# Kernel tuning notes

Measured on AMD Instinct MI355X. Metric: run time of the kernel, lower is better.

## Reference

```python
import jax, jax.numpy as jnp
import numpy as np

S = 1024; VOCAB = 100000; EMB = 300
POS_SZ = 64; CHAR_E = 50; CHAR_ENC = 128; WLEN = 16
NCHARS = 100; NPOSTAG = 50; NPOSITIONS = 1024
D = EMB + 3 * POS_SZ + CHAR_ENC  # word_rep_size = 620
BIH = 128   # per-direction LSTM hidden (bilstm_hidden_size // 2)
TLH = 256; LCC = 128; GCC = 256
NET = 8; NTAGS = 16; NREL = 16
TOKF = 2 * BIH + LCC + TLH       # 640
SENTF = 2 * TOKF + GCC           # 1536

def _p(k, shape):
    return 0.02 * jax.random.normal(k, shape, dtype=jnp.float32)

def setup_inputs():
    key = jax.random.key(0)
    ks = jax.random.split(key, 30)
    return {
        'word_inputs': jax.random.randint(ks[0], (1, S), 0, VOCAB),
        'char_inputs': jax.random.randint(ks[1], (1, S, WLEN), 0, NCHARS),
        'postag_inputs': jax.random.randint(ks[2], (1, S), 0, NPOSTAG),
        'dependency_inputs': jax.random.randint(ks[3], (1, S), 0, 64),
        'position_inputs': jax.random.randint(ks[4], (1, S), 0, NPOSITIONS),
        'topo_order': jnp.arange(S),  # children-before-parents order
        'parent': jnp.concatenate([jnp.arange(1, S), jnp.array([S])]),  # chain dep tree; root -> dummy slot S
        'pointed_token_idx': 5,
        'word_table': _p(ks[5], (VOCAB, EMB)),
        'char_table': _p(ks[6], (NCHARS, CHAR_E)),
        'char_conv_w': _p(ks[7], (CHAR_ENC, CHAR_E, 3)),
        'char_conv_b': jnp.zeros((CHAR_ENC,), jnp.float32),
        'postag_table': _p(ks[8], (NPOSTAG, POS_SZ)),
        'position_table': _p(ks[9], (NPOSITIONS, POS_SZ)),
        'lstm_f_Wx': _p(ks[10], (D, 4 * BIH)),
        'lstm_f_Wh': _p(ks[11], (BIH, 4 * BIH)),
        'lstm_f_b': jnp.zeros((4 * BIH,), jnp.float32),
        'lstm_b_Wx': _p(ks[12], (D, 4 * BIH)),
        'lstm_b_Wh': _p(ks[13], (BIH, 4 * BIH)),
        'lstm_b_b': jnp.zeros((4 * BIH,), jnp.float32),
        'word_cnn_w': _p(ks[14], (LCC, D, 3)),
        'word_cnn_b': jnp.zeros((LCC,), jnp.float32),
        'tl_Wiou': _p(ks[15], (D, 3 * TLH)),
        'tl_Uiou': _p(ks[16], (TLH, 3 * TLH)),
        'tl_biou': jnp.zeros((3 * TLH,), jnp.float32),
        'tl_Wf': _p(ks[17], (D, TLH)),
        'tl_Uf': _p(ks[18], (TLH, TLH)),
        'tl_bf': jnp.zeros((TLH,), jnp.float32),
        'sent_cnn_w': _p(ks[19], (GCC, D, 3)),
        'sent_cnn_b': jnp.zeros((GCC,), jnp.float32),
        'et_w': _p(ks[20], (GCC + TOKF, NET)),
        'et_b': jnp.zeros((NET,), jnp.float32),
        'crf_w': _p(ks[21], (SENTF, NTAGS)),
        'crf_b': jnp.zeros((NTAGS,), jnp.float32),
        'crf_trans': _p(ks[22], (NTAGS, NTAGS)),
        'rel_w': _p(ks[23], (SENTF, NREL)),
        'rel_b': jnp.zeros((NREL,), jnp.float32),
    }

def _conv1d(x, w, b):
    # x: [N, Cin, W], w: [Cout, Cin, K], padding=1 (matches nn.Conv1d(..., padding=1))
    y = jax.lax.conv_general_dilated(x, w, (1,), [(1, 1)], dimension_numbers=('NCW', 'OIW', 'NCW'))
    return y + b[None, :, None]

def _lstm(xs, Wx, Wh, b):
    H = Wh.shape[0]
    def step(carry, x):
        h, c = carry
        g = x @ Wx + h @ Wh + b
        i, f, gg, o = jnp.split(g, 4, axis=-1)
        c = jax.nn.sigmoid(f) * c + jax.nn.sigmoid(i) * jnp.tanh(gg)
        h = jax.nn.sigmoid(o) * jnp.tanh(c)
        return (h, c), h
    init = (jnp.zeros((H,), xs.dtype), jnp.zeros((H,), xs.dtype))
    _, hs = jax.lax.scan(step, init, xs)
    return hs

def _tree_lstm(x, order, parent, Wiou, Uiou, biou, Wf, Uf, bf):
    # ChildSum TreeLSTM over the whole dependency tree in topological order.
    # Equivalent to the source's per-token subtree recursion: each node's h
    # only depends on its subtree.
    Sn, H = x.shape[0], Uf.shape[0]
    xiou = x @ Wiou + biou                 # [S, 3H]
    xf = jnp.concatenate([x @ Wf + bf, jnp.zeros((1, H), x.dtype)], axis=0)  # dummy row for root's parent
    def step(carry, j):
        h, hsum, fcsum = carry
        iou = xiou[j] + hsum[j] @ Uiou
        i, o, u = jnp.split(iou, 3)
        cj = jax.nn.sigmoid(i) * jnp.tanh(u) + fcsum[j]
        hj = jax.nn.sigmoid(o) * jnp.tanh(cj)
        p = parent[j]
        f = jax.nn.sigmoid(xf[p] + hj @ Uf)  # per-child forget gate
        return (h.at[j].set(hj), hsum.at[p].add(hj), fcsum.at[p].add(f * cj)), None
    h0 = jnp.zeros((Sn, H), x.dtype)
    acc0 = jnp.zeros((Sn + 1, H), x.dtype)
    (h, _, _), _ = jax.lax.scan(step, (h0, acc0, acc0), order)
    return h

def _viterbi(emissions, trans):
    # emissions: [S, T]; trans[i, j] = score(i -> j)
    def step(score, e):
        s = score[:, None] + trans
        return jnp.max(s, axis=0) + e, jnp.argmax(s, axis=0)
    final, ptrs = jax.lax.scan(step, emissions[0], emissions[1:])
    last = jnp.argmax(final)
    def bt(tag, p):
        prev = p[tag]
        return prev, prev
    _, prevs = jax.lax.scan(bt, last, ptrs, reverse=True)
    return jnp.concatenate([prevs, last[None]])

def reference(word_inputs, char_inputs, postag_inputs, dependency_inputs, position_inputs, topo_order, parent, pointed_token_idx, word_table, char_table, char_conv_w, char_conv_b, postag_table, position_table, lstm_f_Wx, lstm_f_Wh, lstm_f_b, lstm_b_Wx, lstm_b_Wh, lstm_b_b, word_cnn_w, word_cnn_b, tl_Wiou, tl_Uiou, tl_biou, tl_Wf, tl_Uf, tl_bf, sent_cnn_w, sent_cnn_b, et_w, et_b, crf_w, crf_b, crf_trans, rel_w, rel_b):
    we = word_table[word_inputs]                                   # [1,S,EMB]
    cx = jnp.transpose(char_table[char_inputs[0]], (0, 2, 1))      # [S,CHAR_E,WLEN]
    ce = jnp.max(jax.nn.relu(_conv1d(cx, char_conv_w, char_conv_b)), axis=-1)[None]  # CharCNN -> [1,S,CHAR_ENC]
    pe = postag_table[postag_inputs]
    poe = position_table[position_inputs]
    de = position_table[dependency_inputs]                         # faithful to source bug: uses position table
    inputs = jnp.concatenate([we, ce, pe, poe, de], axis=-1)       # [1,S,D]
    x = inputs[0]
    hf = _lstm(x, lstm_f_Wx, lstm_f_Wh, lstm_f_b)
    hb = _lstm(x[::-1], lstm_b_Wx, lstm_b_Wh, lstm_b_b)[::-1]
    bilstm = jnp.concatenate([hf, hb], axis=-1)[None]              # [1,S,2*BIH]
    xc = jnp.transpose(inputs, (0, 2, 1))                          # [1,D,S]
    local_cnn = jnp.transpose(_conv1d(xc, word_cnn_w, word_cnn_b), (0, 2, 1))
    tree_h = _tree_lstm(x, topo_order, parent, tl_Wiou, tl_Uiou, tl_biou, tl_Wf, tl_Uf, tl_bf)[None]
    global_cnn = jnp.transpose(jnp.max(_conv1d(xc, sent_cnn_w, sent_cnn_b), axis=-1, keepdims=True), (0, 2, 1))  # [1,1,GCC]
    tokens_info = jnp.concatenate([bilstm, local_cnn, tree_h], axis=-1)  # [1,S,TOKF]
    ptr = tokens_info[:, pointed_token_idx, :]                     # [1,TOKF]
    ptr_info = jnp.broadcast_to(ptr[:, None, :], (1, S, TOKF))
    glob_info = jnp.broadcast_to(global_cnn, (1, S, GCC))
    sentence_encoding = jnp.concatenate([tokens_info, ptr_info, glob_info], axis=-1)  # dropout = identity (eval)
    one_vec = jnp.concatenate([global_cnn[:, 0, :], ptr], axis=-1)
    entitytype = jax.nn.softmax(one_vec @ et_w + et_b, axis=-1)
    entities = _viterbi(sentence_encoding[0] @ crf_w + crf_b, crf_trans)
    relations = jax.nn.sigmoid(sentence_encoding @ rel_w + rel_b)
    return sentence_encoding, entitytype, entities, relations
```

## Files before the change

kernel.cpp:

```cpp
#include <hip/hip_runtime.h>
#include <math.h>

#define SEQ   1024
#define DX    620
#define BIH   128
#define TLH   256
#define NTAGS 16

#define O_X      0
#define O_XGF    634880
#define O_XGB    (O_XGF + 524288)
#define O_XIOU   (O_XGB + 524288)
#define O_XF     (O_XIOU + 786432)
#define O_LCNN   (O_XF + 262400)
#define O_SCNN   (O_LCNN + 131072)
#define O_PART   (O_SCNN + 262144)
#define O_GCNN   (O_PART + 4096)
#define O_HF     (O_GCNN + 256)
#define O_HB     (O_HF + 131072)
#define O_TREEH  (O_HB + 131072)
#define O_IOUA   (O_TREEH + 262144)
#define O_FCSUM  (O_IOUA + 787200)
#define O_EMIS   (O_FCSUM + 262400)
#define O_CNT    (O_EMIS + 16384)

#define C_XGF  0
#define C_XGB  16
#define C_XIOU 32
#define C_XF   48
#define C_X    64
#define C_SCNN 80

#define SENT 0xFFFFFFFFu

__device__ __forceinline__ float sig_f(float x){ return 1.0f/(1.0f + __expf(-x)); }
__device__ __forceinline__ float tanh_f(float x){
  float ax = fabsf(x);
  float e  = __expf(-2.0f*ax);
  float t  = (1.0f - e)/(1.0f + e);
  return x < 0.0f ? -t : t;
}
__device__ __forceinline__ int physslot(int s){ return s ^ ((s>>3)&7); }

__device__ __forceinline__ void wait_cnt(int* cnt, int idx, int target){
  while (__hip_atomic_load(&cnt[idx], __ATOMIC_ACQUIRE, __HIP_MEMORY_SCOPE_AGENT) < target)
    __builtin_amdgcn_s_sleep(8);
}

__device__ __forceinline__ void gemm_tile(
    const float* __restrict__ x, const float* __restrict__ Bm,
    const float* __restrict__ bias, float* __restrict__ C,
    int N, int K, int amode, int bx, int by, int tid,
    float (*As)[64], float (*Bs)[64], int agentc)
{
  int bn = bx*64, bm = by*64;
  int lane = tid & 63, kg = tid >> 6;
  int tx = tid & 15, ty = tid >> 4;
  float acc[4][4] = {{0.f}};
  for (int k0 = 0; k0 < K; k0 += 20){
    #pragma unroll
    for (int kk=0; kk<5; kk++){
      int k = kg*5 + kk;
      float av;
      if (amode == 0){
        av = x[(size_t)(bm+lane)*DX + k0 + k];
      } else {
        int kc = k0 + k;
        int d  = kc/3;
        int sh = kc - d*3 - 1;
        int row = bm + lane + sh;
        av = (row >= 0 && row < SEQ) ? x[(size_t)row*DX + d] : 0.0f;
      }
      As[k][lane] = av;
      Bs[k][lane] = (amode==0) ? Bm[(size_t)(k0+k)*N + bn + lane]
                               : Bm[(size_t)(bn+lane)*K + k0 + k];
    }
    __syncthreads();
    #pragma unroll
    for (int k=0;k<20;k++){
      float4 a = *(const float4*)&As[k][ty<<2];
      float4 b = *(const float4*)&Bs[k][tx<<2];
      acc[0][0]+=a.x*b.x; acc[0][1]+=a.x*b.y; acc[0][2]+=a.x*b.z; acc[0][3]+=a.x*b.w;
      acc[1][0]+=a.y*b.x; acc[1][1]+=a.y*b.y; acc[1][2]+=a.y*b.z; acc[1][3]+=a.y*b.w;
      acc[2][0]+=a.z*b.x; acc[2][1]+=a.z*b.y; acc[2][2]+=a.z*b.z; acc[2][3]+=a.z*b.w;
      acc[3][0]+=a.w*b.x; acc[3][1]+=a.w*b.y; acc[3][2]+=a.w*b.z; acc[3][3]+=a.w*b.w;
    }
    __syncthreads();
  }
  float4 bb;
  bb.x = bias[bn+(tx<<2)+0]; bb.y = bias[bn+(tx<<2)+1];
  bb.z = bias[bn+(tx<<2)+2]; bb.w = bias[bn+(tx<<2)+3];
  #pragma unroll
  for (int i=0;i<4;i++){
    int row = bm + (ty<<2) + i;
    float v0 = acc[i][0]+bb.x, v1 = acc[i][1]+bb.y, v2 = acc[i][2]+bb.z, v3 = acc[i][3]+bb.w;
    if (agentc){
      float* p = &C[(size_t)row*N + bn + (tx<<2)];
      __hip_atomic_store(p+0, v0, __ATOMIC_RELAXED, __HIP_MEMORY_SCOPE_AGENT);
      __hip_atomic_store(p+1, v1, __ATOMIC_RELAXED, __HIP_MEMORY_SCOPE_AGENT);
      __hip_atomic_store(p+2, v2, __ATOMIC_RELAXED, __HIP_MEMORY_SCOPE_AGENT);
      __hip_atomic_store(p+3, v3, __ATOMIC_RELAXED, __HIP_MEMORY_SCOPE_AGENT);
    } else {
      float4 o; o.x=v0; o.y=v1; o.z=v2; o.w=v3;
      *(float4*)&C[(size_t)row*N + bn + (tx<<2)] = o;
    }
  }
}

struct RGemm {
  const float* B[4];
  const float* bias[4];
  float*       C[4];
  int          N[4];
};

__global__ __launch_bounds__(256, 1) void k_recur(
    const int* __restrict__ wi, const int* __restrict__ ci,
    const int* __restrict__ postag_in, const int* __restrict__ dep_in, const int* __restrict__ pos_in,
    const float* __restrict__ word_table, const float* __restrict__ char_table,
    const float* __restrict__ ccw, const float* __restrict__ ccb,
    const float* __restrict__ postag_tab, const float* __restrict__ pos_tab,
    const float* __restrict__ xg_f, const float* __restrict__ xg_b,
    const float* __restrict__ Wh_f, const float* __restrict__ Wh_b,
    const float* __restrict__ xiou, const float* __restrict__ xf,
    const float* __restrict__ Uiou, const float* __restrict__ Uf,
    const int* __restrict__ order, const int* __restrict__ parent,
    float* __restrict__ hf, float* __restrict__ hb,
    float* tree_h, float* iou_acc, float* fcsum,
    float* __restrict__ x, RGemm rg_args,
    const float* __restrict__ wcnn_w, const float* __restrict__ wcnn_b,
    const float* __restrict__ scnn_w, const float* __restrict__ scnn_b,
    float* __restrict__ lcnn, float* __restrict__ scnn, float* __restrict__ gcnn,
    int* cnt)
{
  int bid = blockIdx.x;
  int tid = threadIdx.x;

  if (bid >= 775){
    __shared__ __align__(16) float As[20][64];
    __shared__ __align__(16) float Bs[20][64];
    int j = bid - 775;
    for (int s=0;s<3;s++){
      int tn = j*3 + s;
      int by = (tn < 32) ? (tn>>1) : ((tn-32)>>2);
      if (tid == 0){
        int glo = by > 0 ? by-1 : 0, ghi = by < 15 ? by+1 : 15;
        for (int g = glo; g <= ghi; g++) wait_cnt(cnt, C_X + g, 32);
      }
      __syncthreads();
      if (tn < 32){
        gemm_tile(x, wcnn_w, wcnn_b, lcnn, 128, 1860, 1, tn&1, by, tid, As, Bs, 0);
      } else {
        int t2 = tn - 32;
        gemm_tile(x, scnn_w, scnn_b, scnn, 256, 1860, 1, t2&3, by, tid, As, Bs, 0);
        __syncthreads();
        if (tid == 0)
          __hip_atomic_fetch_add(&cnt[C_SCNN], 1, __ATOMIC_RELEASE, __HIP_MEMORY_SCOPE_AGENT);
      }
      __syncthreads();
    }
    return;
  }

  if (bid >= 519){
    __shared__ __align__(16) float As[20][64];
    __shared__ __align__(16) float Bs[20][64];
    int j = bid - 519;
    for (int s=0;s<2;s++){
      int T = j*2 + s;
      int k = T>>5, r = T&31;
      int z, by, bn;
      if (r < 8)       { z=0; by=k;    bn=r;    }
      else if (r < 16) { z=1; by=15-k; bn=r-8;  }
      else if (r < 28) { z=2; by=k;    bn=r-16; }
      else             { z=3; by=k;    bn=r-28; }
      if (tid == 0) wait_cnt(cnt, C_X + by, 32);
      __syncthreads();
      gemm_tile(x, rg_args.B[z], rg_args.bias[z], rg_args.C[z], rg_args.N[z],
                620, 0, bn, by, tid, As, Bs, 1);
      __syncthreads();
      if (tid == 0)
        __hip_atomic_fetch_add(&cnt[z*16 + by], 1, __ATOMIC_RELEASE, __HIP_MEMORY_SCOPE_AGENT);
      __syncthreads();
    }
    return;
  }

  if (bid >= 7){
    int j   = bid - 7;
    int tok = j*2 + (tid >> 7);
    int lt  = tid & 127;
    __shared__ __align__(16) float ce2[2][50][16];
    float (*ce)[16] = ce2[tid >> 7];
    for (int idx = lt; idx < 800; idx += 128){
      int e = idx >> 4, t = idx & 15;
      ce[e][t] = char_table[ci[tok*16 + t]*50 + e];
    }
    __syncthreads();
    float* xr = x + (size_t)tok*DX;
    const float* wrow = word_table + (size_t)wi[tok]*300;
    for (int d = lt; d < 300; d += 128) xr[d] = wrow[d];
    {
      int oc = lt;
      const float* wp = ccw + oc*150;
      float acc[16];
      float b = ccb[oc];
      #pragma unroll
      for (int t=0;t<16;t++) acc[t] = b;
      for (int ic=0; ic<50; ic++){
        float w0 = wp[ic*3+0], w1 = wp[ic*3+1], w2 = wp[ic*3+2];
        float cv[16];
        float4 c0 = *(const float4*)&ce[ic][0];
        float4 c1 = *(const float4*)&ce[ic][4];
        float4 c2 = *(const float4*)&ce[ic][8];
        float4 c3 = *(const float4*)&ce[ic][12];
        cv[0]=c0.x;cv[1]=c0.y;cv[2]=c0.z;cv[3]=c0.w;
        cv[4]=c1.x;cv[5]=c1.y;cv[6]=c1.z;cv[7]=c1.w;
        cv[8]=c2.x;cv[9]=c2.y;cv[10]=c2.z;cv[11]=c2.w;
        cv[12]=c3.x;cv[13]=c3.y;cv[14]=c3.z;cv[15]=c3.w;
        #pragma unroll
        for (int t=0;t<16;t++){
          float a = cv[t]*w1;
          if (t > 0)  a += cv[t-1]*w0;
          if (t < 15) a += cv[t+1]*w2;
          acc[t] += a;
        }
      }
      float m = acc[0];
      #pragma unroll
      for (int t=1;t<16;t++) m = fmaxf(m, acc[t]);
      xr[300 + oc] = fmaxf(m, 0.0f);
    }
    if (lt < 64){
      int d = lt;
      xr[428 + d] = postag_tab[postag_in[tok]*64 + d];
      xr[492 + d] = pos_tab[pos_in[tok]*64 + d];
      xr[556 + d] = pos_tab[dep_in[tok]*64 + d];
    }
    __syncthreads();
    if (tid == 0)
      __hip_atomic_fetch_add(&cnt[C_X + ((j*2) >> 6)], 1, __ATOMIC_RELEASE, __HIP_MEMORY_SCOPE_AGENT);
    return;
  }

  if (bid == 6){
    if (tid == 0) wait_cnt(cnt, C_SCNN, 64);
    __syncthreads();
    int c = tid;
    float m = -3.0e38f;
    #pragma unroll 8
    for (int s = 0; s < SEQ; s++) m = fmaxf(m, scnn[(size_t)s*256 + c]);
    gcnn[c] = m;
    return;
  }

  if (bid >= 4){
    const float* xg  = (bid == 4) ? xg_f : xg_b;
    const float* Wh  = (bid == 4) ? Wh_f : Wh_b;
    float* hout      = (bid == 4) ? hf : hb;
    int zc = (bid == 4) ? 0 : 1;
    int cg = tid >> 1, rg = tid & 1;
    float4 w[4][16];
    #pragma unroll
    for (int cc=0;cc<4;cc++){
      int col = cg*4 + cc;
      #pragma unroll
      for (int r4=0;r4<16;r4++){
        int row = rg*64 + r4*4;
        w[cc][r4].x = Wh[(size_t)(row+0)*512 + col];
        w[cc][r4].y = Wh[(size_t)(row+1)*512 + col];
        w[cc][r4].z = Wh[(size_t)(row+2)*512 + col];
        w[cc][r4].w = Wh[(size_t)(row+3)*512 + col];
      }
    }
    #pragma unroll
    for (int cc=0;cc<4;cc++)
      #pragma unroll
      for (int r4=0;r4<16;r4++)
        asm volatile("" : "+v"(w[cc][r4].x), "+v"(w[cc][r4].y), "+v"(w[cc][r4].z), "+v"(w[cc][r4].w));

    __shared__ __align__(16) float lhl[BIH];
    __shared__ float lcst[BIH];
    __shared__ float gl[512];
    if (tid < BIH){ lhl[tid] = 0.f; lcst[tid] = 0.f; }
    __syncthreads();
    const float4* lhl4 = (const float4*)lhl;

    int Wm = (bid == 4) ? -1 : 16;
    {
      int n0 = (bid == 4) ? 0 : (SEQ-1);
      int g0 = n0 >> 6;
      if (tid == 0){
        if (bid == 4){ for (int g = 0; g <= g0; g++) wait_cnt(cnt, zc*16+g, 8); }
        else         { for (int g = 15; g >= g0; g--) wait_cnt(cnt, zc*16+g, 8); }
      }
      __syncthreads();
      Wm = g0;
    }
    float4 nxg4 = make_float4(0.f,0.f,0.f,0.f);
    if (rg == 0){
      int n0 = (bid == 4) ? 0 : (SEQ-1);
      nxg4 = *(const float4*)&xg[(size_t)n0*512 + cg*4];
    }
    for (int st=0; st<SEQ; st++){
      int n = (bid == 4) ? st : (SEQ-1-st);
      float4 xg4 = nxg4;
      if (st+1 < SEQ){
        int n1 = (bid == 4) ? (st+1) : (SEQ-2-st);
        int g1 = n1 >> 6;
        if (g1 != Wm){
          if (tid == 0) wait_cnt(cnt, zc*16+g1, 8);
          __syncthreads();
          Wm = g1;
        }
        if (rg == 0) nxg4 = *(const float4*)&xg[(size_t)n1*512 + cg*4];
      }
      float acc[4] = {0.f,0.f,0.f,0.f};
      #pragma unroll
      for (int r4=0;r4<16;r4++){
        float4 h4 = lhl4[rg*16 + r4];
        #pragma unroll
        for (int cc=0;cc<4;cc++)
          acc[cc] += h4.x*w[cc][r4].x + h4.y*w[cc][r4].y + h4.z*w[cc][r4].z + h4.w*w[cc][r4].w;
      }
      #pragma unroll
      for (int cc=0;cc<4;cc++) acc[cc] += __shfl_xor(acc[cc], 1);
      if (rg == 0){
        float4 o = make_float4(acc[0]+xg4.x, acc[1]+xg4.y, acc[2]+xg4.z, acc[3]+xg4.w);
        *(float4*)&gl[cg*4] = o;
      }
      __syncthreads();
      if (tid < BIH){
        float gi = gl[tid], gf = gl[BIH+tid], gg = gl[2*BIH+tid], go = gl[3*BIH+tid];
        float c = sig_f(gf)*lcst[tid] + sig_f(gi)*tanh_f(gg);
        float h = sig_f(go)*tanh_f(c);
        lcst[tid] = c;
        lhl[tid] = h;
        hout[(size_t)n*BIH + tid] = h;
      }
      __syncthreads();
    }
    return;
  }

  int blk = bid;
  int cg = tid >> 3, rg = tid & 7;
  int ulo = blk*64;
  float4 w[8][8];
  #pragma unroll
  for (int cc=0;cc<8;cc++){
    int c = cg*8 + cc;
    const float* Wsrc; size_t stride; int gcol;
    if (c < 192){ Wsrc = Uiou; stride = 768; gcol = (c>>6)*TLH + ulo + (c&63); }
    else        { Wsrc = Uf;   stride = 256; gcol = ulo + (c-192); }
    #pragma unroll
    for (int r4=0;r4<8;r4++){
      int row = rg*32 + r4*4;
      w[cc][r4].x = Wsrc[(size_t)(row+0)*stride + gcol];
      w[cc][r4].y = Wsrc[(size_t)(row+1)*stride + gcol];
      w[cc][r4].z = Wsrc[(size_t)(row+2)*stride + gcol];
      w[cc][r4].w = Wsrc[(size_t)(row+3)*stride + gcol];
    }
  }
  #pragma unroll
  for (int cc=0;cc<8;cc++)
    #pragma unroll
    for (int r4=0;r4<8;r4++)
      asm volatile("" : "+v"(w[cc][r4].x), "+v"(w[cc][r4].y), "+v"(w[cc][r4].z), "+v"(w[cc][r4].w));

  __shared__ __align__(16) float hl[TLH];
  __shared__ float colsum[TLH];
  __shared__ float cprev[64];
  __shared__ int ord_l[SEQ];
  __shared__ int par_l[SEQ];
  for (int i=tid; i<SEQ; i+=256){ ord_l[i] = order[i]; par_l[i] = parent[i]; }
  __syncthreads();
  const float4* hl4 = (const float4*)hl;

  int Wm = -1;
  float nxi=0.f, nxo=0.f, nxu=0.f, nxf=0.f;
  {
    int n0 = ord_l[0];
    int need = n0 >> 6;
    if (tid == 0){
      for (int g = 0; g <= need; g++){
        wait_cnt(cnt, C_XIOU + g, 12);
        wait_cnt(cnt, C_XF + g, 4);
      }
    }
    __syncthreads();
    Wm = need;
    if (tid < 64){
      int uu = ulo + tid;
      nxi = xiou[(size_t)n0*768 + uu];
      nxo = xiou[(size_t)n0*768 + 256 + uu];
      nxu = xiou[(size_t)n0*768 + 512 + uu];
    }
  }

  for (int t=0; t<SEQ; t++){
    int n  = ord_l[t];
    int m  = (t > 0) ? ord_l[t-1] : 0;
    int pp = (t > 0) ? par_l[m] : -1;
    bool ppeq = (pp == n);

    int need = -1;
    if (t+1 < SEQ){
      int n1 = ord_l[t+1];
      int pr = par_l[n];
      need = n1 >> 6;
      if (pr < SEQ && (pr>>6) > need) need = pr>>6;
      if (need > Wm){
        if (tid == 0){
          for (int g = Wm+1; g <= need; g++){
            wait_cnt(cnt, C_XIOU + g, 12);
            wait_cnt(cnt, C_XF + g, 4);
          }
        }
        __syncthreads();
        Wm = need;
      }
    }

    float xi=nxi, xo=nxo, xu=nxu, xfv=nxf;
    float ac_i=0.f, ac_o=0.f, ac_u=0.f, fcn=0.f;
    float po_i=0.f, po_o=0.f, po_u=0.f, po_f=0.f;
    if (tid < 64){
      int uu = ulo + tid;
      if (t+1 < SEQ){
        int n1 = ord_l[t+1];
        int pr = par_l[n];
        nxi = xiou[(size_t)n1*768 + uu];
        nxo = xiou[(size_t)n1*768 + 256 + uu];
        nxu = xiou[(size_t)n1*768 + 512 + uu];
        nxf = xf[(size_t)pr*256 + uu];
      }
      ac_i = iou_acc[(size_t)n*768 + uu];
      ac_o = iou_acc[(size_t)n*768 + 256 + uu];
      ac_u = iou_acc[(size_t)n*768 + 512 + uu];
      fcn  = fcsum[(size_t)n*256 + uu];
      if (t > 0 && !ppeq){
        po_i = iou_acc[(size_t)pp*768 + uu];
        po_o = iou_acc[(size_t)pp*768 + 256 + uu];
        po_u = iou_acc[(size_t)pp*768 + 512 + uu];
        po_f = fcsum[(size_t)pp*256 + uu];
      }
    }

    if (t > 0){
      float acc[8] = {0.f,0.f,0.f,0.f,0.f,0.f,0.f,0.f};
      int base = rg << 3;
      #pragma unroll
      for (int r4=0;r4<8;r4++){
        float4 h4 = hl4[base + (r4 ^ rg)];
        #pragma unroll
        for (int cc=0;cc<8;cc++)
          acc[cc] += h4.x*w[cc][r4].x + h4.y*w[cc][r4].y + h4.z*w[cc][r4].z + h4.w*w[cc][r4].w;
      }
      #pragma unroll
      for (int cc=0;cc<8;cc++){
        acc[cc] += __shfl_xor(acc[cc], 1);
        acc[cc] += __shfl_xor(acc[cc], 2);
        acc[cc] += __shfl_xor(acc[cc], 4);
      }
      if (rg == 0){
        *(float4*)&colsum[cg*8]     = make_float4(acc[0], acc[1], acc[2], acc[3]);
        *(float4*)&colsum[cg*8 + 4] = make_float4(acc[4], acc[5], acc[6], acc[7]);
      }
    }
    __syncthreads();

    if (tid < 64){
      int uu = ulo + tid;
      float ai = ac_i, ao = ac_o, au = ac_u, fcs = fcn;
      if (t > 0){
        float vi = colsum[tid], vo = colsum[64+tid], vuu = colsum[128+tid], vf = colsum[192+tid];
        float fg  = sig_f(xfv + vf);
        float fcc = fg * cprev[tid];
        if (ppeq){
          ai += vi; ao += vo; au += vuu; fcs += fcc;
        } else {
          iou_acc[(size_t)pp*768 + uu]       = po_i + vi;
          iou_acc[(size_t)pp*768 + 256 + uu] = po_o + vo;
          iou_acc[(size_t)pp*768 + 512 + uu] = po_u + vuu;
          fcsum[(size_t)pp*256 + uu]         = po_f + fcc;
        }
      }
      float cc = sig_f(xi + ai)*tanh_f(xu + au) + fcs;
      float hh = sig_f(xo + ao)*tanh_f(cc);
      cprev[tid] = cc;
      int s = uu >> 2;
      hl[physslot(s)*4 + (uu & 3)] = hh;
      __hip_atomic_store(&tree_h[(size_t)n*TLH + uu], hh, __ATOMIC_RELAXED, __HIP_MEMORY_SCOPE_AGENT);
    } else if (tid >= 64 && tid < 256){
      int p  = tid - 64;
      int fi = (p < ulo) ? p : p + 64;
      const unsigned* tp = (const unsigned*)(tree_h + (size_t)n*TLH + fi);
      unsigned v = __hip_atomic_load(tp, __ATOMIC_RELAXED, __HIP_MEMORY_SCOPE_AGENT);
      while (v == SENT){
        __builtin_amdgcn_s_sleep(1);
        v = __hip_atomic_load(tp, __ATOMIC_RELAXED, __HIP_MEMORY_SCOPE_AGENT);
      }
      hl[physslot(fi>>2)*4 + (fi&3)] = __uint_as_float(v);
    }
    __syncthreads();
  }
}

__global__ __launch_bounds__(256) void k_assemble(
    const float* __restrict__ hf, const float* __restrict__ hb,
    const float* __restrict__ lcnn, const float* __restrict__ tree_h,
    const float* __restrict__ gcnn,
    const float* __restrict__ crf_w, const float* __restrict__ crf_b,
    const float* __restrict__ rel_w, const float* __restrict__ rel_b,
    const float* __restrict__ et_w, const float* __restrict__ et_b,
    const int* __restrict__ ptk,
    float* __restrict__ se_out, float* __restrict__ emis, float* __restrict__ rel_out,
    float* __restrict__ out_et)
{
  int tid = threadIdx.x;
  int p = ptk[0];
  if (blockIdx.x == SEQ){
    __shared__ float ov[896];
    __shared__ float lg[8];
    for (int d = tid; d < 896; d += 256){
      float v;
      if      (d < 256) v = gcnn[d];
      else if (d < 384) v = hf[(size_t)p*128 + d-256];
      else if (d < 512) v = hb[(size_t)p*128 + d-384];
      else if (d < 640) v = lcnn[(size_t)p*128 + d-512];
      else              v = tree_h[(size_t)p*256 + d-640];
      ov[d] = v;
    }
    __syncthreads();
    int o = tid >> 5, l = tid & 31;
    float a = 0.f;
    for (int k = l; k < 896; k += 32) a += ov[k]*et_w[(size_t)k*8 + o];
    for (int off = 16; off; off >>= 1) a += __shfl_down(a, off, 32);
    if (l == 0) lg[o] = a + et_b[o];
    __syncthreads();
    if (tid == 0){
      float mx = lg[0];
      for (int i=1;i<8;i++) mx = fmaxf(mx, lg[i]);
      float e[8], sum = 0.f;
      for (int i=0;i<8;i++){ e[i] = __expf(lg[i]-mx); sum += e[i]; }
      for (int i=0;i<8;i++) out_et[i] = e[i]/sum;
    }
    return;
  }
  int s = blockIdx.x;
  __shared__ float se[1536];
  for (int d = tid; d < 1536; d += 256){
    float v;
    if      (d < 128)  v = hf[(size_t)s*128 + d];
    else if (d < 256)  v = hb[(size_t)s*128 + d-128];
    else if (d < 384)  v = lcnn[(size_t)s*128 + d-256];
    else if (d < 640)  v = tree_h[(size_t)s*256 + d-384];
    else if (d < 768)  v = hf[(size_t)p*128 + d-640];
    else if (d < 896)  v = hb[(size_t)p*128 + d-768];
    else if (d < 1024) v = lcnn[(size_t)p*128 + d-896];
    else if (d < 1280) v = tree_h[(size_t)p*256 + d-1024];
    else               v = gcnn[d-1280];
    se[d] = v;
    se_out[(size_t)s*1536 + d] = v;
  }
  __syncthreads();
  int o = tid >> 3, l = tid & 7;
  const float* W = (o < 16) ? crf_w : rel_w;
  int oc = (o < 16) ? o : (o - 16);
  float a = 0.f;
  for (int k = l; k < 1536; k += 8) a += se[k]*W[(size_t)k*16 + oc];
  for (int off = 4; off; off >>= 1) a += __shfl_down(a, off, 8);
  if (l == 0){
    if (o < 16) emis[(size_t)s*16 + o] = a + crf_b[o];
    else        rel_out[(size_t)s*16 + oc] = sig_f(a + rel_b[oc]);
  }
}

__global__ __launch_bounds__(64) void k_viterbi(
    const float* __restrict__ emis, const float* __restrict__ trans, float* __restrict__ out_e)
{
  __shared__ __align__(16) float ring[64][16];
  __shared__ unsigned char ptrs[1023*16];
  __shared__ float scL[16];
  int l = threadIdx.x;
  int j = l >> 2, iq = l & 3;
  float tr0 = trans[(iq*4+0)*16 + j];
  float tr1 = trans[(iq*4+1)*16 + j];
  float tr2 = trans[(iq*4+2)*16 + j];
  float tr3 = trans[(iq*4+3)*16 + j];
  {
    const float* src = &emis[(size_t)l*16];
    float4 a = *(const float4*)(src+0), b = *(const float4*)(src+4);
    float4 c = *(const float4*)(src+8), d = *(const float4*)(src+12);
    *(float4*)&ring[l][0] = a;  *(float4*)&ring[l][4] = b;
    *(float4*)&ring[l][8] = c;  *(float4*)&ring[l][12] = d;
  }
  float cur = ring[0][j];
  float sc0 = __shfl(cur, (iq*4+0)<<2, 64);
  float sc1 = __shfl(cur, (iq*4+1)<<2, 64);
  float sc2 = __shfl(cur, (iq*4+2)<<2, 64);
  float sc3 = __shfl(cur, (iq*4+3)<<2, 64);
  float myfinal = cur;
  for (int t=1; t<1024; t++){
    if ((t & 63) == 0){
      const float* src = &emis[(size_t)(t+l)*16];
      float4 a = *(const float4*)(src+0), b = *(const float4*)(src+4);
      float4 c = *(const float4*)(src+8), d = *(const float4*)(src+12);
      int rr = (t+l) & 63;
      *(float4*)&ring[rr][0] = a;  *(float4*)&ring[rr][4] = b;
      *(float4*)&ring[rr][8] = c;  *(float4*)&ring[rr][12] = d;
    }
    float v0 = sc0 + tr0, v1 = sc1 + tr1, v2 = sc2 + tr2, v3 = sc3 + tr3;
    float best = v0; int barg = iq*4;
    if (v1 > best){ best = v1; barg = iq*4+1; }
    if (v2 > best){ best = v2; barg = iq*4+2; }
    if (v3 > best){ best = v3; barg = iq*4+3; }
    float ob = __shfl_down(best, 1, 4); int oa = __shfl_down(barg, 1, 4);
    if (ob > best){ best = ob; barg = oa; }
    ob = __shfl_down(best, 2, 4); oa = __shfl_down(barg, 2, 4);
    if (ob > best){ best = ob; barg = oa; }
    float ns = 0.f;
    if (iq == 0){
      ns = best + ring[t & 63][j];
      ptrs[(t-1)*16 + j] = (unsigned char)barg;
      myfinal = ns;
    }
    sc0 = __shfl(ns, (iq*4+0)<<2, 64);
    sc1 = __shfl(ns, (iq*4+1)<<2, 64);
    sc2 = __shfl(ns, (iq*4+2)<<2, 64);
    sc3 = __shfl(ns, (iq*4+3)<<2, 64);
  }
  if (iq == 0) scL[j] = myfinal;
  if (l == 0){
    float b = scL[0]; int last = 0;
    #pragma unroll
    for (int i=1;i<16;i++){ if (scL[i] > b){ b = scL[i]; last = i; } }
    out_e[1023] = (float)last;
    int cur2 = last;
    for (int t=1022; t>=0; t--){ cur2 = (int)ptrs[t*16 + cur2]; out_e[t] = (float)cur2; }
  }
}

extern "C" void kernel_launch(void* const* d_in, const int* in_sizes, int n_in,
                              void* d_out, int out_size, void* d_ws, size_t ws_size,
                              hipStream_t stream)
{
  (void)in_sizes; (void)n_in; (void)out_size; (void)ws_size;
  const int*   wi         = (const int*)d_in[0];
  const int*   ci         = (const int*)d_in[1];
  const int*   postag_in  = (const int*)d_in[2];
  const int*   dep_in     = (const int*)d_in[3];
  const int*   pos_in     = (const int*)d_in[4];
  const int*   order      = (const int*)d_in[5];
  const int*   parent     = (const int*)d_in[6];
  const int*   ptk        = (const int*)d_in[7];
  const float* word_table = (const float*)d_in[8];
  const float* char_table = (const float*)d_in[9];
  const float* ccw        = (const float*)d_in[10];
  const float* ccb        = (const float*)d_in[11];
  const float* postag_tab = (const float*)d_in[12];
  const float* pos_tab    = (const float*)d_in[13];
  const float* Wx_f       = (const float*)d_in[14];
  const float* Wh_f       = (const float*)d_in[15];
  const float* b_f        = (const float*)d_in[16];
  const float* Wx_b       = (const float*)d_in[17];
  const float* Wh_b       = (const float*)d_in[18];
  const float* b_b        = (const float*)d_in[19];
  const float* wcnn_w     = (const float*)d_in[20];
  const float* wcnn_b     = (const float*)d_in[21];
  const float* Wiou       = (const float*)d_in[22];
  const float* Uiou       = (const float*)d_in[23];
  const float* biou       = (const float*)d_in[24];
  const float* Wf_t       = (const float*)d_in[25];
  const float* Uf_t       = (const float*)d_in[26];
  const float* bf_t       = (const float*)d_in[27];
  const float* scnn_w     = (const float*)d_in[28];
  const float* scnn_b     = (const float*)d_in[29];
  const float* et_w       = (const float*)d_in[30];
  const float* et_b       = (const float*)d_in[31];
  const float* crf_w      = (const float*)d_in[32];
  const float* crf_b      = (const float*)d_in[33];
  const float* crf_trans  = (const float*)d_in[34];
  const float* rel_w      = (const float*)d_in[35];
  const float* rel_b      = (const float*)d_in[36];

  float* ws = (float*)d_ws;
  float* x      = ws + O_X;
  float* xg_f   = ws + O_XGF;
  float* xg_b   = ws + O_XGB;
  float* xiou   = ws + O_XIOU;
  float* xf     = ws + O_XF;
  float* lcnn   = ws + O_LCNN;
  float* scnn   = ws + O_SCNN;
  float* gcnn   = ws + O_GCNN;
  float* hf     = ws + O_HF;
  float* hb     = ws + O_HB;
  float* tree_h = ws + O_TREEH;
  float* iou_acc= ws + O_IOUA;
  float* fcsum  = ws + O_FCSUM;
  float* emis   = ws + O_EMIS;
  int*   cnt    = (int*)(ws + O_CNT);

  float* outF     = (float*)d_out;
  float* se_out   = outF;
  float* et_out   = outF + 1572864;
  float* ent_out  = outF + 1572872;
  float* rel_out  = outF + 1573896;

  hipMemsetAsync(xf, 0, (size_t)1025*256*sizeof(float), stream);
  hipMemsetAsync(iou_acc, 0, ((size_t)1025*768 + 1025*256)*sizeof(float), stream);
  hipMemsetAsync(tree_h, 0xFF, (size_t)1024*256*sizeof(float), stream);
  hipMemsetAsync(cnt, 0, 512, stream);

  RGemm rga;
  rga.B[0]=Wx_f;  rga.bias[0]=b_f;   rga.C[0]=xg_f; rga.N[0]=512;
  rga.B[1]=Wx_b;  rga.bias[1]=b_b;   rga.C[1]=xg_b; rga.N[1]=512;
  rga.B[2]=Wiou;  rga.bias[2]=biou;  rga.C[2]=xiou; rga.N[2]=768;
  rga.B[3]=Wf_t;  rga.bias[3]=bf_t;  rga.C[3]=xf;   rga.N[3]=256;

  k_recur<<<807, 256, 0, stream>>>(wi, ci, postag_in, dep_in, pos_in,
                                   word_table, char_table, ccw, ccb,
                                   postag_tab, pos_tab,
                                   xg_f, xg_b, Wh_f, Wh_b, xiou, xf, Uiou, Uf_t,
                                   order, parent, hf, hb, tree_h, iou_acc, fcsum,
                                   x, rga, wcnn_w, wcnn_b, scnn_w, scnn_b,
                                   lcnn, scnn, gcnn, cnt);

  k_assemble<<<SEQ+1, 256, 0, stream>>>(hf, hb, lcnn, tree_h, gcnn,
                                        crf_w, crf_b, rel_w, rel_b, et_w, et_b, ptk,
                                        se_out, emis, rel_out, et_out);

  k_viterbi<<<1, 64, 0, stream>>>(emis, crf_trans, ent_out);
}
```

Baseline: 2.787 ms.

## Split embedding into separate kernel launched before the recurrent megakernel

Moves the token-embedding and char-CNN work out of the persistent k_recur megakernel into its own k_embed launch that runs first. This removes the per-row-group counters and spin-waits that GEMM and CNN blocks used to wait for x, and shrinks the megakernel grid from 807 to 295 blocks. In exchange it adds a kernel launch boundary and serialises embedding ahead of the recurrences, so the LSTM can no longer start while embeddings are still being produced. It also contains some cleanup, such as dropping a dead Wm initialiser and simplifying a thread branch.

```diff
diff --git a/kernel.cpp b/kernel.cpp
--- a/kernel.cpp
+++ b/kernel.cpp
@@ -24,12 +24,7 @@
 #define O_EMIS   (O_FCSUM + 262400)
 #define O_CNT    (O_EMIS + 16384)
 
-#define C_XGF  0
-#define C_XGB  16
-#define C_XIOU 32
-#define C_XF   48
-#define C_X    64
-#define C_SCNN 80
+#define C_SCNN 64
 
 #define SENT 0xFFFFFFFFu
 
@@ -45,6 +40,64 @@
 __device__ __forceinline__ void wait_cnt(int* cnt, int idx, int target){
   while (__hip_atomic_load(&cnt[idx], __ATOMIC_ACQUIRE, __HIP_MEMORY_SCOPE_AGENT) < target)
     __builtin_amdgcn_s_sleep(8);
+}
+
+__global__ __launch_bounds__(128) void k_embed(
+    const int* __restrict__ wi, const int* __restrict__ ci,
+    const int* __restrict__ postag_in, const int* __restrict__ dep_in, const int* __restrict__ pos_in,
+    const float* __restrict__ word_table, const float* __restrict__ char_table,
+    const float* __restrict__ ccw, const float* __restrict__ ccb,
+    const float* __restrict__ postag_table, const float* __restrict__ position_table,
+    float* __restrict__ x)
+{
+  int s = blockIdx.x;
+  int tid = threadIdx.x;
+  __shared__ __align__(16) float ce[50][16];
+  for (int idx = tid; idx < 800; idx += 128){
+    int e = idx >> 4, t = idx & 15;
+    ce[e][t] = char_table[ci[s*16 + t]*50 + e];
+  }
+  __syncthreads();
+  float* xr = x + (size_t)s*DX;
+  const float* wrow = word_table + (size_t)wi[s]*300;
+  for (int d = tid; d < 300; d += 128) xr[d] = wrow[d];
+  {
+    int oc = tid;
+    const float* wp = ccw + oc*150;
+    float acc[16];
+    float b = ccb[oc];
+    #pragma unroll
+    for (int t=0;t<16;t++) acc[t] = b;
+    for (int ic=0; ic<50; ic++){
+      float w0 = wp[ic*3+0], w1 = wp[ic*3+1], w2 = wp[ic*3+2];
+      float cv[16];
+      float4 c0 = *(const float4*)&ce[ic][0];
+      float4 c1 = *(const float4*)&ce[ic][4];
+      float4 c2 = *(const float4*)&ce[ic][8];
+      float4 c3 = *(const float4*)&ce[ic][12];
+      cv[0]=c0.x;cv[1]=c0.y;cv[2]=c0.z;cv[3]=c0.w;
+      cv[4]=c1.x;cv[5]=c1.y;cv[6]=c1.z;cv[7]=c1.w;
+      cv[8]=c2.x;cv[9]=c2.y;cv[10]=c2.z;cv[11]=c2.w;
+      cv[12]=c3.x;cv[13]=c3.y;cv[14]=c3.z;cv[15]=c3.w;
+      #pragma unroll
+      for (int t=0;t<16;t++){
+        float a = cv[t]*w1;
+        if (t > 0)  a += cv[t-1]*w0;
+        if (t < 15) a += cv[t+1]*w2;
+        acc[t] += a;
+      }
+    }
+    float m = acc[0];
+    #pragma unroll
+    for (int t=1;t<16;t++) m = fmaxf(m, acc[t]);
+    xr[300 + oc] = fmaxf(m, 0.0f);
+  }
+  if (tid < 64){
+    int d = tid;
+    xr[428 + d] = postag_table[postag_in[s]*64 + d];
+    xr[492 + d] = position_table[pos_in[s]*64 + d];
+    xr[556 + d] = position_table[dep_in[s]*64 + d];
+  }
 }
 
 __device__ __forceinline__ void gemm_tile(
@@ -115,11 +168,6 @@
 };
 
 __global__ __launch_bounds__(256, 1) void k_recur(
-    const int* __restrict__ wi, const int* __restrict__ ci,
-    const int* __restrict__ postag_in, const int* __restrict__ dep_in, const int* __restrict__ pos_in,
-    const float* __restrict__ word_table, const float* __restrict__ char_table,
-    const float* __restrict__ ccw, const float* __restrict__ ccb,
-    const float* __restrict__ postag_tab, const float* __restrict__ pos_tab,
     const float* __restrict__ xg_f, const float* __restrict__ xg_b,
     const float* __restrict__ Wh_f, const float* __restrict__ Wh_b,
     const float* __restrict__ xiou, const float* __restrict__ xf,
@@ -127,7 +175,7 @@
     const int* __restrict__ order, const int* __restrict__ parent,
     float* __restrict__ hf, float* __restrict__ hb,
     float* tree_h, float* iou_acc, float* fcsum,
-    float* __restrict__ x, RGemm rg_args,
+    const float* __restrict__ x, RGemm rg_args,
     const float* __restrict__ wcnn_w, const float* __restrict__ wcnn_b,
     const float* __restrict__ scnn_w, const float* __restrict__ scnn_b,
     float* __restrict__ lcnn, float* __restrict__ scnn, float* __restrict__ gcnn,
@@ -136,23 +184,28 @@
   int bid = blockIdx.x;
   int tid = threadIdx.x;
 
-  if (bid >= 775){
+  if (bid == 294){
+    if (tid == 0) wait_cnt(cnt, C_SCNN, 64);
+    __syncthreads();
+    int c = tid;
+    float m = -3.0e38f;
+    #pragma unroll 8
+    for (int s = 0; s < SEQ; s++) m = fmaxf(m, scnn[(size_t)s*256 + c]);
+    gcnn[c] = m;
+    return;
+  }
+
+  if (bid >= 262){
     __shared__ __align__(16) float As[20][64];
     __shared__ __align__(16) float Bs[20][64];
-    int j = bid - 775;
+    int j = bid - 262;
     for (int s=0;s<3;s++){
       int tn = j*3 + s;
-      int by = (tn < 32) ? (tn>>1) : ((tn-32)>>2);
-      if (tid == 0){
-        int glo = by > 0 ? by-1 : 0, ghi = by < 15 ? by+1 : 15;
-        for (int g = glo; g <= ghi; g++) wait_cnt(cnt, C_X + g, 32);
-      }
-      __syncthreads();
       if (tn < 32){
-        gemm_tile(x, wcnn_w, wcnn_b, lcnn, 128, 1860, 1, tn&1, by, tid, As, Bs, 0);
+        gemm_tile(x, wcnn_w, wcnn_b, lcnn, 128, 1860, 1, tn&1, tn>>1, tid, As, Bs, 0);
       } else {
-        int t2 = tn - 32;
-        gemm_tile(x, scnn_w, scnn_b, scnn, 256, 1860, 1, t2&3, by, tid, As, Bs, 0);
+        int t2 = tn-32;
+        gemm_tile(x, scnn_w, scnn_b, scnn, 256, 1860, 1, t2&3, t2>>2, tid, As, Bs, 0);
         __syncthreads();
         if (tid == 0)
           __hip_atomic_fetch_add(&cnt[C_SCNN], 1, __ATOMIC_RELEASE, __HIP_MEMORY_SCOPE_AGENT);
@@ -162,10 +215,10 @@
     return;
   }
 
-  if (bid >= 519){
+  if (bid >= 6){
     __shared__ __align__(16) float As[20][64];
     __shared__ __align__(16) float Bs[20][64];
-    int j = bid - 519;
+    int j = bid - 6;
     for (int s=0;s<2;s++){
       int T = j*2 + s;
       int k = T>>5, r = T&31;
@@ -174,8 +227,6 @@
       else if (r < 16) { z=1; by=15-k; bn=r-8;  }
       else if (r < 28) { z=2; by=k;    bn=r-16; }
       else             { z=3; by=k;    bn=r-28; }
-      if (tid == 0) wait_cnt(cnt, C_X + by, 32);
-      __syncthreads();
       gemm_tile(x, rg_args.B[z], rg_args.bias[z], rg_args.C[z], rg_args.N[z],
                 620, 0, bn, by, tid, As, Bs, 1);
       __syncthreads();
@@ -183,74 +234,6 @@
         __hip_atomic_fetch_add(&cnt[z*16 + by], 1, __ATOMIC_RELEASE, __HIP_MEMORY_SCOPE_AGENT);
       __syncthreads();
     }
-    return;
-  }
-
-  if (bid >= 7){
-    int j   = bid - 7;
-    int tok = j*2 + (tid >> 7);
-    int lt  = tid & 127;
-    __shared__ __align__(16) float ce2[2][50][16];
-    float (*ce)[16] = ce2[tid >> 7];
-    for (int idx = lt; idx < 800; idx += 128){
-      int e = idx >> 4, t = idx & 15;
-      ce[e][t] = char_table[ci[tok*16 + t]*50 + e];
-    }
-    __syncthreads();
-    float* xr = x + (size_t)tok*DX;
-    const float* wrow = word_table + (size_t)wi[tok]*300;
-    for (int d = lt; d < 300; d += 128) xr[d] = wrow[d];
-    {
-      int oc = lt;
-      const float* wp = ccw + oc*150;
-      float acc[16];
-      float b = ccb[oc];
-      #pragma unroll
-      for (int t=0;t<16;t++) acc[t] = b;
-      for (int ic=0; ic<50; ic++){
-        float w0 = wp[ic*3+0], w1 = wp[ic*3+1], w2 = wp[ic*3+2];
-        float cv[16];
-        float4 c0 = *(const float4*)&ce[ic][0];
-        float4 c1 = *(const float4*)&ce[ic][4];
-        float4 c2 = *(const float4*)&ce[ic][8];
-        float4 c3 = *(const float4*)&ce[ic][12];
-        cv[0]=c0.x;cv[1]=c0.y;cv[2]=c0.z;cv[3]=c0.w;
-        cv[4]=c1.x;cv[5]=c1.y;cv[6]=c1.z;cv[7]=c1.w;
-        cv[8]=c2.x;cv[9]=c2.y;cv[10]=c2.z;cv[11]=c2.w;
-        cv[12]=c3.x;cv[13]=c3.y;cv[14]=c3.z;cv[15]=c3.w;
-        #pragma unroll
-        for (int t=0;t<16;t++){
-          float a = cv[t]*w1;
-          if (t > 0)  a += cv[t-1]*w0;
-          if (t < 15) a += cv[t+1]*w2;
-          acc[t] += a;
-        }
-      }
-      float m = acc[0];
-      #pragma unroll
-      for (int t=1;t<16;t++) m = fmaxf(m, acc[t]);
-      xr[300 + oc] = fmaxf(m, 0.0f);
-    }
-    if (lt < 64){
-      int d = lt;
-      xr[428 + d] = postag_tab[postag_in[tok]*64 + d];
-      xr[492 + d] = pos_tab[pos_in[tok]*64 + d];
-      xr[556 + d] = pos_tab[dep_in[tok]*64 + d];
-    }
-    __syncthreads();
-    if (tid == 0)
-      __hip_atomic_fetch_add(&cnt[C_X + ((j*2) >> 6)], 1, __ATOMIC_RELEASE, __HIP_MEMORY_SCOPE_AGENT);
-    return;
-  }
-
-  if (bid == 6){
-    if (tid == 0) wait_cnt(cnt, C_SCNN, 64);
-    __syncthreads();
-    int c = tid;
-    float m = -3.0e38f;
-    #pragma unroll 8
-    for (int s = 0; s < SEQ; s++) m = fmaxf(m, scnn[(size_t)s*256 + c]);
-    gcnn[c] = m;
     return;
   }
 
@@ -286,7 +269,7 @@
     __syncthreads();
     const float4* lhl4 = (const float4*)lhl;
 
-    int Wm = (bid == 4) ? -1 : 16;
+    int Wm;
     {
       int n0 = (bid == 4) ? 0 : (SEQ-1);
       int g0 = n0 >> 6;
@@ -384,8 +367,8 @@
     int need = n0 >> 6;
     if (tid == 0){
       for (int g = 0; g <= need; g++){
-        wait_cnt(cnt, C_XIOU + g, 12);
-        wait_cnt(cnt, C_XF + g, 4);
+        wait_cnt(cnt, 32 + g, 12);
+        wait_cnt(cnt, 48 + g, 4);
       }
     }
     __syncthreads();
@@ -404,17 +387,16 @@
     int pp = (t > 0) ? par_l[m] : -1;
     bool ppeq = (pp == n);
 
-    int need = -1;
     if (t+1 < SEQ){
       int n1 = ord_l[t+1];
       int pr = par_l[n];
-      need = n1 >> 6;
+      int need = n1 >> 6;
       if (pr < SEQ && (pr>>6) > need) need = pr>>6;
       if (need > Wm){
         if (tid == 0){
           for (int g = Wm+1; g <= need; g++){
-            wait_cnt(cnt, C_XIOU + g, 12);
-            wait_cnt(cnt, C_XF + g, 4);
+            wait_cnt(cnt, 32 + g, 12);
+            wait_cnt(cnt, 48 + g, 4);
           }
         }
         __syncthreads();
@@ -492,7 +474,7 @@
       int s = uu >> 2;
       hl[physslot(s)*4 + (uu & 3)] = hh;
       __hip_atomic_store(&tree_h[(size_t)n*TLH + uu], hh, __ATOMIC_RELAXED, __HIP_MEMORY_SCOPE_AGENT);
-    } else if (tid >= 64 && tid < 256){
+    } else {
       int p  = tid - 64;
       int fi = (p < ulo) ? p : p + 64;
       const unsigned* tp = (const unsigned*)(tree_h + (size_t)n*TLH + fi);
@@ -713,16 +695,17 @@
   hipMemsetAsync(tree_h, 0xFF, (size_t)1024*256*sizeof(float), stream);
   hipMemsetAsync(cnt, 0, 512, stream);
 
+  k_embed<<<SEQ, 128, 0, stream>>>(wi, ci, postag_in, dep_in, pos_in,
+                                   word_table, char_table, ccw, ccb,
+                                   postag_tab, pos_tab, x);
+
   RGemm rga;
   rga.B[0]=Wx_f;  rga.bias[0]=b_f;   rga.C[0]=xg_f; rga.N[0]=512;
   rga.B[1]=Wx_b;  rga.bias[1]=b_b;   rga.C[1]=xg_b; rga.N[1]=512;
   rga.B[2]=Wiou;  rga.bias[2]=biou;  rga.C[2]=xiou; rga.N[2]=768;
   rga.B[3]=Wf_t;  rga.bias[3]=bf_t;  rga.C[3]=xf;   rga.N[3]=256;
 
-  k_recur<<<807, 256, 0, stream>>>(wi, ci, postag_in, dep_in, pos_in,
-                                   word_table, char_table, ccw, ccb,
-                                   postag_tab, pos_tab,
-                                   xg_f, xg_b, Wh_f, Wh_b, xiou, xf, Uiou, Uf_t,
+  k_recur<<<295, 256, 0, stream>>>(xg_f, xg_b, Wh_f, Wh_b, xiou, xf, Uiou, Uf_t,
                                    order, parent, hf, hb, tree_h, iou_acc, fcsum,
                                    x, rga, wcnn_w, wcnn_b, scnn_w, scnn_b,
                                    lcnn, scnn, gcnn, cnt);
```

New measurement: 2.760 ms. Within noise of the previous version (-0.9%).
